# Optimization experiments

Measured on AMD Instinct MI355X. Metric: run time of the kernel, lower is better.

Reference implementation:

```python
import jax, jax.numpy as jnp
import numpy as np

IMG = 640.0
CONF_THRE = 0.05
NMS_THRE = 0.5
MAX_DET = 100          # fixed NMS output slots (padded with zeros / valid-masked)
PRE_NMS_TOPK = 1000    # candidates kept before NMS
NEG = -1e9
CLS_OFFSET = 4096.0    # batched_nms class-offset trick (> max coordinate)


def _make_anchors():
    # YOLO-style grid anchors: 3 scales per location, strides 8/16/32 -> N = 25200
    levels = []
    for s in (8, 16, 32):
        g = int(IMG) // s
        c = (np.arange(g, dtype=np.float32) + 0.5) * s
        cy, cx = np.meshgrid(c, c, indexing="ij")
        cx, cy = cx.reshape(-1), cy.reshape(-1)
        for scale in (0.5, 1.0, 2.0):
            w = s * 4.0 * scale
            levels.append(np.stack([cx - w / 2, cy - w / 2, cx + w / 2, cy + w / 2], 1))
    return np.concatenate(levels, 0).astype(np.float32)  # [25200, 4]


def setup_inputs() -> dict:
    key = jax.random.key(0)
    k1, k2 = jax.random.split(key)
    B, N, C = 16, 25200, 80
    return {
        "proposals_regs": jax.random.uniform(k1, (B, N, 5), dtype=jnp.float32),
        "proposals_clses": jax.random.uniform(k2, (B, N, C), dtype=jnp.float32),
        "anchors": jnp.asarray(_make_anchors()),
    }


def _decode(deltas, anchors):
    # standard delta decode relative to anchors, then clip to image (clip_bboxes)
    aw = anchors[:, 2] - anchors[:, 0]
    ah = anchors[:, 3] - anchors[:, 1]
    acx = (anchors[:, 0] + anchors[:, 2]) * 0.5
    acy = (anchors[:, 1] + anchors[:, 3]) * 0.5
    cx = acx + deltas[:, 0] * aw
    cy = acy + deltas[:, 1] * ah
    w = aw * jnp.exp(deltas[:, 2])
    h = ah * jnp.exp(deltas[:, 3])
    boxes = jnp.stack([cx - w / 2, cy - h / 2, cx + w / 2, cy + h / 2], 1)
    return jnp.clip(boxes, 0.0, IMG)


def _iou_one(box, boxes):
    lt = jnp.maximum(box[:2], boxes[:, :2])
    rb = jnp.minimum(box[2:], boxes[:, 2:])
    wh = jnp.clip(rb - lt, 0.0)
    inter = wh[:, 0] * wh[:, 1]
    a = (box[2] - box[0]) * (box[3] - box[1])
    b = (boxes[:, 2] - boxes[:, 0]) * (boxes[:, 3] - boxes[:, 1])
    union = a + b - inter
    return jnp.where(union > 0, inter / union, 0.0)


def _nms(boxes, scores):
    # greedy hard NMS with fixed MAX_DET iterations (jit-safe, fixed shapes)
    def body(i, st):
        sc, keep, ks = st
        best = jnp.argmax(sc)
        keep = keep.at[i].set(best.astype(jnp.int32))
        ks = ks.at[i].set(sc[best])
        sc = jnp.where(_iou_one(boxes[best], boxes) > NMS_THRE, NEG, sc)
        sc = sc.at[best].set(NEG)
        return sc, keep, ks
    keep0 = jnp.zeros((MAX_DET,), jnp.int32)
    ks0 = jnp.full((MAX_DET,), NEG, scores.dtype)
    _, keep, ks = jax.lax.fori_loop(0, MAX_DET, body, (scores, keep0, ks0))
    return keep, ks


def _per_image(reg, cls, anchors):
    p_obj = reg[:, 4]
    boxes = _decode(reg[:, :4], anchors)                     # [N,4] clipped xyxy
    class_conf = jnp.max(cls, axis=1)
    class_pred = jax.lax.stop_gradient(jnp.argmax(cls, axis=1))
    scores = p_obj * class_conf                              # batched_nms score
    scores = jnp.where(scores >= CONF_THRE, scores, NEG)     # confidence mask
    top_s, top_i = jax.lax.top_k(scores, PRE_NMS_TOPK)
    b = boxes[top_i]
    cp = class_pred[top_i].astype(boxes.dtype)
    obj = p_obj[top_i]
    cc = class_conf[top_i]
    off_boxes = b + cp[:, None] * CLS_OFFSET                 # per-class NMS
    keep, kept_scores = _nms(off_boxes, top_s)
    valid = kept_scores > NEG * 0.5
    det = jnp.concatenate(
        [b[keep], obj[keep][:, None], cc[keep][:, None], cp[keep][:, None]], 1
    )  # [MAX_DET, 7] = x1,y1,x2,y2,obj,conf,cls (same layout as torch code)
    return jnp.where(valid[:, None], det, 0.0)


def reference(proposals_regs, proposals_clses, anchors):
    return jax.vmap(lambda r, c: _per_image(r, c, anchors))(
        proposals_regs, proposals_clses
    )  # [B, MAX_DET, 7]
```

## Files before the change

kernel.cpp:

```cpp
#include <hip/hip_runtime.h>
#include <math.h>

#define BB 16
#define NN 25200
#define NCLS 80
#define TOPK 1000
#define MAXDET 100
#define CAND_CAP 2048
#define RANKS 1024
#define HBINS 1024
#define HBASE 0xBD00u
#define BPI_C 99
static constexpr float NEGV = -1000000000.0f;
static constexpr float IMGSZ = 640.0f;

struct Meta {
  unsigned b1p;
  unsigned b1c;
  unsigned b1;
  unsigned n_true;
  unsigned cnt;
  unsigned pad0, pad1, pad2;
};

__device__ __forceinline__ unsigned flipKey(float f) {
  unsigned u = __float_as_uint(f);
  return (u & 0x80000000u) ? ~u : (u | 0x80000000u);
}
__device__ __forceinline__ float unflipKey(unsigned k) {
  unsigned u = (k & 0x80000000u) ? (k & 0x7FFFFFFFu) : ~k;
  return __uint_as_float(u);
}

__global__ void __launch_bounds__(256) k_zero(unsigned* __restrict__ p) {
  p[blockIdx.x * 256 + threadIdx.x] = 0u;
}

__global__ void __launch_bounds__(256) k_pobj(const float* __restrict__ regs,
                                              unsigned* __restrict__ pkey,
                                              unsigned* __restrict__ histp) {
  int g = blockIdx.x * 256 + threadIdx.x;
  float pobj = regs[(size_t)g * 5 + 4];
  unsigned key = flipKey(pobj);
  pkey[g] = key;
  if (pobj >= 0.05f)
    atomicAdd(&histp[(size_t)(g / NN) * HBINS + ((key >> 16) - HBASE)], 1u);
}

__global__ void __launch_bounds__(256) k_scan(const unsigned* __restrict__ hist,
                                              Meta* __restrict__ meta, int mode) {
  __shared__ unsigned part[256];
  __shared__ unsigned sfx[256];
  __shared__ int s_sel;
  __shared__ unsigned s_cum;
  int img = blockIdx.x;
  int t = threadIdx.x;
  const unsigned* h = hist + (size_t)img * HBINS;
  uint4 mine = reinterpret_cast<const uint4*>(h)[t];
  unsigned s = mine.x + mine.y + mine.z + mine.w;
  if (t == 0) { s_sel = -1; s_cum = 0; }
  part[t] = s;
  sfx[t] = s;
  __syncthreads();
  for (int d = 1; d < 256; d <<= 1) {
    unsigned v = (t + d < 256) ? sfx[t + d] : 0u;
    __syncthreads();
    sfx[t] += v;
    __syncthreads();
  }
  {
    unsigned incl = sfx[t];
    unsigned excl = incl - part[t];
    if (incl >= (unsigned)TOPK && excl < (unsigned)TOPK) { s_sel = t; s_cum = excl; }
  }
  __syncthreads();
  unsigned total = sfx[0];
  if (total < (unsigned)TOPK) {
    if (t == 0) {
      if (mode == 0) meta[img].b1p = HBASE + 1;
      else if (mode == 1) meta[img].b1c = HBASE + 1;
      else { meta[img].b1 = HBASE + 1; meta[img].n_true = total; }
    }
  } else if (t == s_sel) {
    unsigned cum = s_cum;
    unsigned vals[4] = {mine.x, mine.y, mine.z, mine.w};
    int sel = 0;
    unsigned c_ge = 0;
    for (int j = 3; j >= 0; --j) {
      if (cum + vals[j] >= (unsigned)TOPK) { sel = j; c_ge = cum + vals[j]; break; }
      cum += vals[j];
    }
    unsigned bin = HBASE + (unsigned)(4 * t + sel);
    if (mode == 0) meta[img].b1p = bin;
    else if (mode == 1) meta[img].b1c = bin;
    else {
      meta[img].b1 = bin;
      meta[img].n_true = (c_ge > (unsigned)TOPK) ? (unsigned)TOPK : c_ge;
    }
  }
}

__global__ void __launch_bounds__(256) k_cand(const float* __restrict__ regs,
                                              const float* __restrict__ clses,
                                              const unsigned* __restrict__ pkey,
                                              const Meta* __restrict__ meta,
                                              unsigned* __restrict__ keys,
                                              float* __restrict__ ccs,
                                              int* __restrict__ preds,
                                              unsigned* __restrict__ hists, int mode) {
  int g = blockIdx.x * 256 + threadIdx.x;
  int img = g / NN;
  unsigned pk = pkey[g];
  unsigned pk16 = pk >> 16;
  unsigned lo = (mode == 0) ? meta[img].b1p : meta[img].b1c;
  unsigned hi = (mode == 0) ? 0x10000u : meta[img].b1p;
  if (pk16 < lo || pk16 >= hi) return;
  const float4* r4 = reinterpret_cast<const float4*>(clses + (size_t)g * NCLS);
  float best = -1.0f;
  int bi = 0;
#pragma unroll
  for (int f = 0; f < 20; ++f) {
    float4 v = r4[f];
    int b0 = f * 4;
    if (v.x > best) { best = v.x; bi = b0 + 0; }
    if (v.y > best) { best = v.y; bi = b0 + 1; }
    if (v.z > best) { best = v.z; bi = b0 + 2; }
    if (v.w > best) { best = v.w; bi = b0 + 3; }
  }
  float pobj = unflipKey(pk);
  float sc = pobj * best;
  bool pass = (sc >= 0.05f);
  unsigned key = flipKey(pass ? sc : NEGV);
  keys[g] = key;
  ccs[g] = best;
  preds[g] = bi;
  if (pass) atomicAdd(&hists[(size_t)img * HBINS + ((key >> 16) - HBASE)], 1u);
}

__global__ void k_compact(const float* __restrict__ regs, const float* __restrict__ anchors,
                          const unsigned* __restrict__ keys, const float* __restrict__ ccs,
                          const int* __restrict__ preds, Meta* __restrict__ meta,
                          float* __restrict__ cand) {
  const size_t S2 = (size_t)BB * CAND_CAP;
  int img = blockIdx.x / BPI_C;
  int i = (blockIdx.x % BPI_C) * 256 + threadIdx.x;
  if (i >= NN) return;
  int lane = threadIdx.x & 63;
  unsigned long long lt = (1ull << lane) - 1ull;
  size_t g = (size_t)img * NN + (size_t)i;
  unsigned key = keys[g];
  bool take = (key >> 16) >= meta[img].b1;
  unsigned long long mA = __ballot(take);
  if (!take) return;
  int leader = __builtin_ctzll(mA);
  unsigned base = 0;
  if (lane == leader) base = atomicAdd(&meta[img].cnt, (unsigned)__popcll(mA));
  base = __shfl(base, leader);
  unsigned pos = base + (unsigned)__popcll(mA & lt);
  if (pos >= CAND_CAP) return;
  const float* r = regs + g * 5;
  float d0 = r[0], d1 = r[1], d2 = r[2], d3 = r[3], obj = r[4];
  const float* a = anchors + (size_t)i * 4;
  float ax1 = a[0], ay1 = a[1], ax2 = a[2], ay2 = a[3];
  float aw = ax2 - ax1, ah = ay2 - ay1;
  float acx = (ax1 + ax2) * 0.5f, acy = (ay1 + ay2) * 0.5f;
  float cx = acx + d0 * aw, cy = acy + d1 * ah;
  float w = aw * expf(d2), h = ah * expf(d3);
  float hw = 0.5f * w, hh = 0.5f * h;
  float x1 = fminf(fmaxf(cx - hw, 0.0f), IMGSZ);
  float y1 = fminf(fmaxf(cy - hh, 0.0f), IMGSZ);
  float x2 = fminf(fmaxf(cx + hw, 0.0f), IMGSZ);
  float y2 = fminf(fmaxf(cy + hh, 0.0f), IMGSZ);
  size_t o = (size_t)img * CAND_CAP + pos;
  cand[0 * S2 + o] = x1;
  cand[1 * S2 + o] = y1;
  cand[2 * S2 + o] = x2;
  cand[3 * S2 + o] = y2;
  cand[4 * S2 + o] = obj;
  cand[5 * S2 + o] = ccs[g];
  cand[6 * S2 + o] = (float)preds[g];
  cand[7 * S2 + o] = unflipKey(key);
  reinterpret_cast<unsigned*>(cand + 8 * S2)[o] = (unsigned)i;
}

__global__ void __launch_bounds__(256) k_rank(const float* __restrict__ cand,
                                              const Meta* __restrict__ meta,
                                              float* __restrict__ boxr,
                                              float4* __restrict__ payr0,
                                              float4* __restrict__ payr1) {
  const size_t S2 = (size_t)BB * CAND_CAP;
  const int NR = BB * RANKS;
  __shared__ unsigned long long kk[CAND_CAP];
  int img = blockIdx.x >> 5;
  int part = blockIdx.x & 31;
  int tid = threadIdx.x;
  unsigned nload = meta[img].cnt;
  if (nload > CAND_CAP) nload = CAND_CAP;
  for (int i = tid; i < CAND_CAP; i += 256) {
    unsigned long long kv = 0ull;
    if (i < (int)nload) {
      float sc = cand[7 * S2 + (size_t)img * CAND_CAP + i];
      unsigned ai = reinterpret_cast<const unsigned*>(cand + 8 * S2)[(size_t)img * CAND_CAP + i];
      kv = ((unsigned long long)flipKey(sc) << 16) |
           (unsigned long long)((0x7FFFu - ai) & 0xFFFFu);
    }
    kk[i] = kv;
  }
  __syncthreads();
  int slot = part * 64 + (tid >> 2);
  int qtr = tid & 3;
  unsigned long long myk = kk[slot];
  unsigned rank = 0;
  for (int q = qtr * 512; q < qtr * 512 + 512; ++q) rank += (kk[q] > myk) ? 1u : 0u;
  rank += (unsigned)__builtin_amdgcn_update_dpp(0, (int)rank, 0xB1, 0xF, 0xF, true);
  rank += (unsigned)__builtin_amdgcn_update_dpp(0, (int)rank, 0x4E, 0xF, 0xF, true);
  if (qtr == 0 && slot < (int)nload && rank < RANKS) {
    size_t o = (size_t)img * CAND_CAP + slot;
    float x1 = cand[0 * S2 + o], y1 = cand[1 * S2 + o];
    float x2 = cand[2 * S2 + o], y2 = cand[3 * S2 + o];
    float obj = cand[4 * S2 + o], cc = cand[5 * S2 + o];
    float cp = cand[6 * S2 + o], sc = cand[7 * S2 + o];
    float offv = cp * 4096.0f;
    float a1 = x1 + offv, b1v = y1 + offv, a2 = x2 + offv, b2v = y2 + offv;
    size_t ro = (size_t)img * RANKS + rank;
    boxr[0 * NR + ro] = a1;
    boxr[1 * NR + ro] = b1v;
    boxr[2 * NR + ro] = a2;
    boxr[3 * NR + ro] = b2v;
    boxr[4 * NR + ro] = (a2 - a1) * (b2v - b1v);
    payr0[ro] = make_float4(x1, y1, x2, y2);
    payr1[ro] = make_float4(obj, cc, cp, sc);
  }
}

__global__ void __launch_bounds__(256) k_matrix(const float* __restrict__ boxr,
                                                const Meta* __restrict__ meta,
                                                unsigned long long* __restrict__ mat) {
  const int NR = BB * RANKS;
  __shared__ float sx1[RANKS], sy1[RANKS], sx2[RANKS], sy2[RANKS], sar[RANKS];
  int img = blockIdx.x >> 6;
  int part = blockIdx.x & 63;
  int tid = threadIdx.x, lane = tid & 63, wid = tid >> 6;
  for (int i = tid; i < RANKS; i += 256) {
    int g = img * RANKS + i;
    sx1[i] = boxr[0 * NR + g];
    sy1[i] = boxr[1 * NR + g];
    sx2[i] = boxr[2 * NR + g];
    sy2[i] = boxr[3 * NR + g];
    sar[i] = boxr[4 * NR + g];
  }
  unsigned n = meta[img].n_true;
  __syncthreads();
#pragma unroll
  for (int rr = 0; rr < 4; ++rr) {
    int r = part * 16 + wid * 4 + rr;
    if (r >= (int)n) continue;
    float bx1 = sx1[r], by1 = sy1[r], bx2 = sx2[r], by2 = sy2[r], bA = sar[r];
    unsigned long long* rowp = mat + ((size_t)img * RANKS + r) * 16;
#pragma unroll
    for (int w2 = 0; w2 < 16; ++w2) {
      int c = w2 * 64 + lane;
      float lx = fmaxf(bx1, sx1[c]), ly = fmaxf(by1, sy1[c]);
      float rx = fminf(bx2, sx2[c]), ry = fminf(by2, sy2[c]);
      float iw = fmaxf(rx - lx, 0.f), ih = fmaxf(ry - ly, 0.f);
      float inter = iw * ih;
      float uu = bA + sar[c] - inter;
      float ss = fmaf(2.0f, inter, -uu);
      float tt = uu * 0x1p-24f;
      bool sup = (uu > 0.f && ss > tt) || (c == r);
      unsigned long long b = __ballot(sup);
      if (lane == w2) rowp[w2] = b;
    }
  }
}

__global__ void __launch_bounds__(256, 1) k_scan2(const unsigned long long* __restrict__ mat,
                                                  const Meta* __restrict__ meta,
                                                  const float4* __restrict__ payr0,
                                                  const float4* __restrict__ payr1,
                                                  float* __restrict__ out) {
  __shared__ unsigned long long smat[RANKS * 16];
  __shared__ unsigned wins[MAXDET];
  __shared__ float4 lout4[MAXDET * 7 / 4];
  int img = blockIdx.x, tid = threadIdx.x, lane = tid & 63, wid = tid >> 6;
  const uint4* gm = reinterpret_cast<const uint4*>(mat + (size_t)img * RANKS * 16);
  uint4* sm4 = reinterpret_cast<uint4*>(smat);
  for (int i = tid; i < RANKS * 16 / 2; i += 256) sm4[i] = gm[i];
  if (tid < MAXDET) wins[tid] = 0xFFFFFFFFu;
  unsigned n = meta[img].n_true;
  __syncthreads();
  if (wid == 0) {
    unsigned long long alive = 0ull;
    if (lane < 16) {
      int lo = lane * 64;
      alive = ((int)n >= lo + 64) ? ~0ull
                                  : (((int)n > lo) ? ((1ull << ((int)n - lo)) - 1ull) : 0ull);
    }
    for (int it = 0; it < MAXDET; ++it) {
      unsigned long long any = __ballot(alive != 0ull);
      if (any == 0ull) break;
      int f = __builtin_ctzll(any);
      unsigned long long w = __shfl(alive, f);
      int r = f * 64 + __builtin_ctzll(w);
      if (lane == 0) wins[it] = (unsigned)r;
      unsigned long long rowv = (lane < 16) ? smat[r * 16 + lane] : 0ull;
      alive &= ~rowv;
    }
  }
  __syncthreads();
  if (tid < MAXDET) {
    unsigned r = wins[tid];
    float* row = reinterpret_cast<float*>(lout4) + tid * 7;
    if (r == 0xFFFFFFFFu) {
      row[0] = 0.f; row[1] = 0.f; row[2] = 0.f; row[3] = 0.f;
      row[4] = 0.f; row[5] = 0.f; row[6] = 0.f;
    } else {
      float4 p0 = payr0[(size_t)img * RANKS + r];
      float4 p1 = payr1[(size_t)img * RANKS + r];
      row[0] = p0.x; row[1] = p0.y; row[2] = p0.z; row[3] = p0.w;
      row[4] = p1.x; row[5] = p1.y; row[6] = p1.z;
    }
  }
  __syncthreads();
  float4* go4 = reinterpret_cast<float4*>(out + (size_t)img * MAXDET * 7);
  if (tid < MAXDET * 7 / 4) go4[tid] = lout4[tid];
}

extern "C" void kernel_launch(void* const* d_in, const int* in_sizes, int n_in,
                              void* d_out, int out_size, void* d_ws, size_t ws_size,
                              hipStream_t stream) {
  const float* regs = (const float*)d_in[0];
  const float* clses = (const float*)d_in[1];
  const float* anchors = (const float*)d_in[2];
  float* out = (float*)d_out;
  char* ws = (char*)d_ws;

  constexpr size_t HISTP_OFF = 0;
  constexpr size_t HISTS_OFF = 65536;
  constexpr size_t META_OFF = 131072;
  constexpr size_t KEYS_OFF = 132096;
  constexpr size_t ARR_BYTES = (size_t)BB * NN * 4;
  constexpr size_t ZERO_BYTES = KEYS_OFF + ARR_BYTES;
  constexpr size_t CCS_OFF = KEYS_OFF + ARR_BYTES;
  constexpr size_t PREDS_OFF = CCS_OFF + ARR_BYTES;
  constexpr size_t PKEY_OFF = PREDS_OFF + ARR_BYTES;
  constexpr size_t CAND_OFF = PKEY_OFF + ARR_BYTES;
  constexpr size_t CAND_BYTES = (size_t)9 * BB * CAND_CAP * 4;
  constexpr size_t BOXR_OFF = CAND_OFF + CAND_BYTES;
  constexpr size_t BOXR_BYTES = (size_t)5 * BB * RANKS * 4;
  constexpr size_t PAYR_OFF = BOXR_OFF + BOXR_BYTES;
  constexpr size_t PAYR_BYTES = (size_t)2 * BB * RANKS * 16;
  constexpr size_t MAT_OFF = PAYR_OFF + PAYR_BYTES;

  unsigned* histp = (unsigned*)(ws + HISTP_OFF);
  unsigned* hists = (unsigned*)(ws + HISTS_OFF);
  Meta* meta = (Meta*)(ws + META_OFF);
  unsigned* keys = (unsigned*)(ws + KEYS_OFF);
  float* ccs = (float*)(ws + CCS_OFF);
  int* preds = (int*)(ws + PREDS_OFF);
  unsigned* pkey = (unsigned*)(ws + PKEY_OFF);
  float* cand = (float*)(ws + CAND_OFF);
  float* boxr = (float*)(ws + BOXR_OFF);
  float4* payr0 = (float4*)(ws + PAYR_OFF);
  float4* payr1 = (float4*)(ws + PAYR_OFF + (size_t)BB * RANKS * 16);
  unsigned long long* mat = (unsigned long long*)(ws + MAT_OFF);

  k_zero<<<(int)(ZERO_BYTES / 1024), 256, 0, stream>>>((unsigned*)ws);

  int rblocks = BB * NN / 256;
  k_pobj<<<rblocks, 256, 0, stream>>>(regs, pkey, histp);
  k_scan<<<BB, 256, 0, stream>>>(histp, meta, 0);
  k_cand<<<rblocks, 256, 0, stream>>>(regs, clses, pkey, meta, keys, ccs, preds, hists, 0);
  k_scan<<<BB, 256, 0, stream>>>(hists, meta, 1);
  k_cand<<<rblocks, 256, 0, stream>>>(regs, clses, pkey, meta, keys, ccs, preds, hists, 1);
  k_scan<<<BB, 256, 0, stream>>>(hists, meta, 2);
  k_compact<<<BB * BPI_C, 256, 0, stream>>>(regs, anchors, keys, ccs, preds, meta, cand);
  k_rank<<<BB * 32, 256, 0, stream>>>(cand, meta, boxr, payr0, payr1);
  k_matrix<<<BB * 64, 256, 0, stream>>>(boxr, meta, mat);
  k_scan2<<<BB, 256, 0, stream>>>(mat, meta, payr0, payr1, out);
}
```

Baseline: 154.6 us.

## Fuse candidate compaction into k_cand and drop intermediate key/class arrays

The separate compaction kernel and the full-size keys/ccs/preds intermediate arrays are removed. k_cand now writes every passing candidate straight into the compact candidate buffer, using a per-thread atomic counter and decoding the box inline. The zeroed workspace shrinks to the small header region. Because k_cand covers a wider score band than the final threshold bin, the candidate capacity doubles to 4096, so the rank kernel now does twice the comparisons per element and launches twice as many blocks. Per-thread atomics on a single counter per image could contend.

```diff
diff --git a/kernel.cpp b/kernel.cpp
--- a/kernel.cpp
+++ b/kernel.cpp
@@ -6,11 +6,10 @@
 #define NCLS 80
 #define TOPK 1000
 #define MAXDET 100
-#define CAND_CAP 2048
+#define CAND_CAP 4096
 #define RANKS 1024
 #define HBINS 1024
 #define HBASE 0xBD00u
-#define BPI_C 99
 static constexpr float NEGV = -1000000000.0f;
 static constexpr float IMGSZ = 640.0f;
 
@@ -102,12 +101,12 @@
 
 __global__ void __launch_bounds__(256) k_cand(const float* __restrict__ regs,
                                               const float* __restrict__ clses,
+                                              const float* __restrict__ anchors,
                                               const unsigned* __restrict__ pkey,
-                                              const Meta* __restrict__ meta,
-                                              unsigned* __restrict__ keys,
-                                              float* __restrict__ ccs,
-                                              int* __restrict__ preds,
+                                              Meta* __restrict__ meta,
+                                              float* __restrict__ cand,
                                               unsigned* __restrict__ hists, int mode) {
+  const size_t S2 = (size_t)BB * CAND_CAP;
   int g = blockIdx.x * 256 + threadIdx.x;
   int img = g / NN;
   unsigned pk = pkey[g];
@@ -129,36 +128,12 @@
   }
   float pobj = unflipKey(pk);
   float sc = pobj * best;
-  bool pass = (sc >= 0.05f);
-  unsigned key = flipKey(pass ? sc : NEGV);
-  keys[g] = key;
-  ccs[g] = best;
-  preds[g] = bi;
-  if (pass) atomicAdd(&hists[(size_t)img * HBINS + ((key >> 16) - HBASE)], 1u);
-}
-
-__global__ void k_compact(const float* __restrict__ regs, const float* __restrict__ anchors,
-                          const unsigned* __restrict__ keys, const float* __restrict__ ccs,
-                          const int* __restrict__ preds, Meta* __restrict__ meta,
-                          float* __restrict__ cand) {
-  const size_t S2 = (size_t)BB * CAND_CAP;
-  int img = blockIdx.x / BPI_C;
-  int i = (blockIdx.x % BPI_C) * 256 + threadIdx.x;
-  if (i >= NN) return;
-  int lane = threadIdx.x & 63;
-  unsigned long long lt = (1ull << lane) - 1ull;
-  size_t g = (size_t)img * NN + (size_t)i;
-  unsigned key = keys[g];
-  bool take = (key >> 16) >= meta[img].b1;
-  unsigned long long mA = __ballot(take);
-  if (!take) return;
-  int leader = __builtin_ctzll(mA);
-  unsigned base = 0;
-  if (lane == leader) base = atomicAdd(&meta[img].cnt, (unsigned)__popcll(mA));
-  base = __shfl(base, leader);
-  unsigned pos = base + (unsigned)__popcll(mA & lt);
+  if (sc < 0.05f) return;
+  atomicAdd(&hists[(size_t)img * HBINS + ((flipKey(sc) >> 16) - HBASE)], 1u);
+  unsigned pos = atomicAdd(&meta[img].cnt, 1u);
   if (pos >= CAND_CAP) return;
-  const float* r = regs + g * 5;
+  int i = g - img * NN;
+  const float* r = regs + (size_t)g * 5;
   float d0 = r[0], d1 = r[1], d2 = r[2], d3 = r[3], obj = r[4];
   const float* a = anchors + (size_t)i * 4;
   float ax1 = a[0], ay1 = a[1], ax2 = a[2], ay2 = a[3];
@@ -177,9 +152,9 @@
   cand[2 * S2 + o] = x2;
   cand[3 * S2 + o] = y2;
   cand[4 * S2 + o] = obj;
-  cand[5 * S2 + o] = ccs[g];
-  cand[6 * S2 + o] = (float)preds[g];
-  cand[7 * S2 + o] = unflipKey(key);
+  cand[5 * S2 + o] = best;
+  cand[6 * S2 + o] = (float)bi;
+  cand[7 * S2 + o] = sc;
   reinterpret_cast<unsigned*>(cand + 8 * S2)[o] = (unsigned)i;
 }
 
@@ -191,8 +166,8 @@
   const size_t S2 = (size_t)BB * CAND_CAP;
   const int NR = BB * RANKS;
   __shared__ unsigned long long kk[CAND_CAP];
-  int img = blockIdx.x >> 5;
-  int part = blockIdx.x & 31;
+  int img = blockIdx.x >> 6;
+  int part = blockIdx.x & 63;
   int tid = threadIdx.x;
   unsigned nload = meta[img].cnt;
   if (nload > CAND_CAP) nload = CAND_CAP;
@@ -211,7 +186,7 @@
   int qtr = tid & 3;
   unsigned long long myk = kk[slot];
   unsigned rank = 0;
-  for (int q = qtr * 512; q < qtr * 512 + 512; ++q) rank += (kk[q] > myk) ? 1u : 0u;
+  for (int q = qtr * 1024; q < qtr * 1024 + 1024; ++q) rank += (kk[q] > myk) ? 1u : 0u;
   rank += (unsigned)__builtin_amdgcn_update_dpp(0, (int)rank, 0xB1, 0xF, 0xF, true);
   rank += (unsigned)__builtin_amdgcn_update_dpp(0, (int)rank, 0x4E, 0xF, 0xF, true);
   if (qtr == 0 && slot < (int)nload && rank < RANKS) {
@@ -338,12 +313,9 @@
   constexpr size_t HISTP_OFF = 0;
   constexpr size_t HISTS_OFF = 65536;
   constexpr size_t META_OFF = 131072;
-  constexpr size_t KEYS_OFF = 132096;
+  constexpr size_t ZERO_BYTES = 132096;
+  constexpr size_t PKEY_OFF = ZERO_BYTES;
   constexpr size_t ARR_BYTES = (size_t)BB * NN * 4;
-  constexpr size_t ZERO_BYTES = KEYS_OFF + ARR_BYTES;
-  constexpr size_t CCS_OFF = KEYS_OFF + ARR_BYTES;
-  constexpr size_t PREDS_OFF = CCS_OFF + ARR_BYTES;
-  constexpr size_t PKEY_OFF = PREDS_OFF + ARR_BYTES;
   constexpr size_t CAND_OFF = PKEY_OFF + ARR_BYTES;
   constexpr size_t CAND_BYTES = (size_t)9 * BB * CAND_CAP * 4;
   constexpr size_t BOXR_OFF = CAND_OFF + CAND_BYTES;
@@ -355,9 +327,6 @@
   unsigned* histp = (unsigned*)(ws + HISTP_OFF);
   unsigned* hists = (unsigned*)(ws + HISTS_OFF);
   Meta* meta = (Meta*)(ws + META_OFF);
-  unsigned* keys = (unsigned*)(ws + KEYS_OFF);
-  float* ccs = (float*)(ws + CCS_OFF);
-  int* preds = (int*)(ws + PREDS_OFF);
   unsigned* pkey = (unsigned*)(ws + PKEY_OFF);
   float* cand = (float*)(ws + CAND_OFF);
   float* boxr = (float*)(ws + BOXR_OFF);
@@ -370,12 +339,11 @@
   int rblocks = BB * NN / 256;
   k_pobj<<<rblocks, 256, 0, stream>>>(regs, pkey, histp);
   k_scan<<<BB, 256, 0, stream>>>(histp, meta, 0);
-  k_cand<<<rblocks, 256, 0, stream>>>(regs, clses, pkey, meta, keys, ccs, preds, hists, 0);
+  k_cand<<<rblocks, 256, 0, stream>>>(regs, clses, anchors, pkey, meta, cand, hists, 0);
   k_scan<<<BB, 256, 0, stream>>>(hists, meta, 1);
-  k_cand<<<rblocks, 256, 0, stream>>>(regs, clses, pkey, meta, keys, ccs, preds, hists, 1);
+  k_cand<<<rblocks, 256, 0, stream>>>(regs, clses, anchors, pkey, meta, cand, hists, 1);
   k_scan<<<BB, 256, 0, stream>>>(hists, meta, 2);
-  k_compact<<<BB * BPI_C, 256, 0, stream>>>(regs, anchors, keys, ccs, preds, meta, cand);
-  k_rank<<<BB * 32, 256, 0, stream>>>(cand, meta, boxr, payr0, payr1);
+  k_rank<<<BB * 64, 256, 0, stream>>>(cand, meta, boxr, payr0, payr1);
   k_matrix<<<BB * 64, 256, 0, stream>>>(boxr, meta, mat);
   k_scan2<<<BB, 256, 0, stream>>>(mat, meta, payr0, payr1, out);
 }
```

New measurement: 271.3 us. 75.6% more time.
